# Kernel optimization log

Hardware: AMD Instinct MI355X
Metric: run time of the kernel (lower is better)

Reference implementation:

```python
import jax, jax.numpy as jnp
import numpy as np

S, D, H, DI, DV, DFF = 2048, 1024, 16, 64, 64, 4096


def _xavier(k, shape):
    fan_in, fan_out = shape[-2], shape[-1]
    lim = float(np.sqrt(6.0 / (fan_in + fan_out)))
    return jax.random.uniform(k, shape, jnp.float32, -lim, lim)


def setup_inputs() -> dict:
    key = jax.random.key(0)
    ks = jax.random.split(key, 8)
    input_vecs = jax.random.normal(ks[0], (S, D), jnp.float32)
    WQs = _xavier(ks[1], (H, D, DI))
    WKs = _xavier(ks[2], (H, D, DI))
    WVs = _xavier(ks[3], (H, D, DV))
    WO_w = _xavier(ks[4], (D, H * DV))   # torch Linear weight [out, in]
    WO_b = jnp.zeros((D,), jnp.float32)
    FF1_w = _xavier(ks[5], (DFF, D))
    FF1_b = jnp.zeros((DFF,), jnp.float32)
    FF2_w = _xavier(ks[6], (D, DFF))
    FF2_b = jnp.zeros((D,), jnp.float32)
    return dict(input_vecs=input_vecs, WQs=WQs, WKs=WKs, WVs=WVs,
                WO_w=WO_w, WO_b=WO_b, FF1_w=FF1_w, FF1_b=FF1_b,
                FF2_w=FF2_w, FF2_b=FF2_b)


def reference(input_vecs, WQs, WKs, WVs, WO_w, WO_b, FF1_w, FF1_b, FF2_w, FF2_b):
    h, _, di = WQs.shape
    s = input_vecs.shape[0]
    # per-head projections: [h, s, di/dv]
    Q = jnp.einsum('sd,hde->hse', input_vecs, WQs)
    K = jnp.einsum('sd,hde->hse', input_vecs, WKs)
    V = jnp.einsum('sd,hdv->hsv', input_vecs, WVs)
    scores = jnp.einsum('hse,hte->hst', Q, K) / jnp.sqrt(jnp.float32(di))
    # ALiBi bias: slope_h = (2^{-8/H})^h for h = 1..H; bias = -max(0, i-j)*slope
    idx = jnp.arange(s)
    delta = idx[:, None] - idx[None, :]               # [s, s], i - j
    slopes = (2.0 ** (-8.0 / h)) ** jnp.arange(1, h + 1, dtype=jnp.float32)
    bias = -jnp.maximum(delta, 0).astype(jnp.float32) * slopes[:, None, None]
    causal_mask = jnp.where(delta < 0, -jnp.inf, 0.0)  # -inf above diagonal
    SA = jax.nn.softmax(scores + bias + causal_mask, axis=-1)  # [h, s, s]
    z = jnp.einsum('hst,htv->hsv', SA, V)
    # hstack over heads == transpose to [s, h, dv] then flatten
    zconcat = jnp.transpose(z, (1, 0, 2)).reshape(s, -1)
    attouts = input_vecs + zconcat @ WO_w.T + WO_b
    output_vecs = attouts + jax.nn.relu(attouts @ FF1_w.T + FF1_b) @ FF2_w.T + FF2_b
    return SA, output_vecs
```

## Files before the change

kernel.cpp:

```cpp
#include <hip/hip_runtime.h>
#include <hip/hip_bf16.h>

typedef __hip_bfloat16 bf16;
typedef short v8s __attribute__((ext_vector_type(8)));
typedef float f32x4 __attribute__((ext_vector_type(4)));

static constexpr int S = 2048, D = 1024, H = 16, DFF = 4096;

__device__ __forceinline__ bf16  f2b(float x) { return __float2bfloat16(x); }
__device__ __forceinline__ float b2f(bf16 x)  { return __bfloat162float(x); }

__device__ __forceinline__ void gl2lds16(const void* g, void* l) {
    __builtin_amdgcn_global_load_lds(
        (const __attribute__((address_space(1))) unsigned int*)g,
        (__attribute__((address_space(3))) unsigned int*)l, 16, 0, 0);
}

__global__ __launch_bounds__(256)
void cvt_all(const float* __restrict__ X, const float* __restrict__ WO,
             const float* __restrict__ F1, const float* __restrict__ F2,
             bf16* __restrict__ Xb, bf16* __restrict__ WOb,
             bf16* __restrict__ F1b, bf16* __restrict__ F2b)
{
    const float* src; bf16* dst; int n4;
    switch (blockIdx.y) {
        case 0:  src = X;  dst = Xb;  n4 = S * D / 4;   break;
        case 1:  src = WO; dst = WOb; n4 = D * D / 4;   break;
        case 2:  src = F1; dst = F1b; n4 = DFF * D / 4; break;
        default: src = F2; dst = F2b; n4 = D * DFF / 4; break;
    }
    const int i = blockIdx.x * 256 + threadIdx.x;
    if (i < n4) {
        const float4 v = ((const float4*)src)[i];
        bf16* p = dst + (size_t)i * 4;
        p[0] = f2b(v.x); p[1] = f2b(v.y); p[2] = f2b(v.z); p[3] = f2b(v.w);
    }
}

__global__ __launch_bounds__(256)
void pack_w(const float* __restrict__ WQ, const float* __restrict__ WK,
            const float* __restrict__ WV, bf16* __restrict__ Wcat)
{
    const int d0 = blockIdx.x * 64, h = blockIdx.y, sel = blockIdx.z;
    const float* W = (sel == 0) ? WQ : (sel == 1) ? WK : WV;
    __shared__ float t[64][65];
    const int tid = threadIdx.x;
    for (int idx = tid; idx < 4096; idx += 256) {
        const int d = idx >> 6, e = idx & 63;
        t[d][e] = W[((size_t)h * D + d0 + d) * 64 + e];
    }
    __syncthreads();
    for (int idx = tid; idx < 4096; idx += 256) {
        const int e = idx >> 6, d = idx & 63;
        Wcat[(size_t)(sel * 1024 + h * 64 + e) * D + d0 + d] = f2b(t[d][e]);
    }
}

template<int EPI>
__global__ __launch_bounds__(256)
void gemm_nt(const bf16* __restrict__ A, const bf16* __restrict__ B,
             int M, int N, int K,
             const float* __restrict__ bias, const float* __restrict__ res_f,
             float* __restrict__ out_f, bf16* __restrict__ out_h,
             bf16* __restrict__ Qb, bf16* __restrict__ Kb, bf16* __restrict__ Vt)
{
    __shared__ bf16 sA[128 * 32];
    __shared__ bf16 sB[128 * 32];
    const int tid = threadIdx.x;
    const int lane = tid & 63, quad = lane >> 4, l15 = lane & 15;
    const int wave = tid >> 6, wm = wave >> 1, wn = wave & 1;
    const size_t m0 = (size_t)blockIdx.x * 128, n0 = (size_t)blockIdx.y * 128;
    const int trow = tid >> 2, tcol = (tid & 3) * 8;

    const bf16* pA = A + (m0 + trow) * (size_t)K + tcol;
    const bf16* pB = B + (n0 + trow) * (size_t)K + tcol;
    bf16* lA = sA + tid * 8;
    bf16* lB = sB + tid * 8;

    f32x4 acc[4][4] = {};

    for (int k0 = 0; k0 < K; k0 += 32) {
        gl2lds16(pA + k0, lA);
        gl2lds16(pA + 64 * (size_t)K + k0, lA + 2048);
        gl2lds16(pB + k0, lB);
        gl2lds16(pB + 64 * (size_t)K + k0, lB + 2048);
        __syncthreads();
        v8s af[4], bfr[4];
        #pragma unroll
        for (int t = 0; t < 4; ++t) {
            af[t]  = *(const v8s*)(sA + (wm * 64 + t * 16 + l15) * 32 + quad * 8);
            bfr[t] = *(const v8s*)(sB + (wn * 64 + t * 16 + l15) * 32 + quad * 8);
        }
        #pragma unroll
        for (int i = 0; i < 4; ++i)
            #pragma unroll
            for (int j = 0; j < 4; ++j)
                acc[i][j] = __builtin_amdgcn_mfma_f32_16x16x32_bf16(af[i], bfr[j], acc[i][j], 0, 0, 0);
        __syncthreads();
    }

    #pragma unroll
    for (int i = 0; i < 4; ++i) {
        const size_t mbase = m0 + wm * 64 + i * 16 + quad * 4;
        #pragma unroll
        for (int j = 0; j < 4; ++j) {
            const size_t n = n0 + wn * 64 + j * 16 + l15;
            if constexpr (EPI == 0) {
                const int sel = (int)(n >> 10), hh = (int)((n >> 6) & 15), e = (int)(n & 63);
                if (sel == 2) {
                    bf16* p = Vt + ((size_t)hh * 64 + e) * S + mbase;
                    p[0] = f2b(acc[i][j][0]); p[1] = f2b(acc[i][j][1]);
                    p[2] = f2b(acc[i][j][2]); p[3] = f2b(acc[i][j][3]);
                } else {
                    const float sc = (sel == 0) ? 0.125f : 1.0f;
                    bf16* p = ((sel == 0) ? Qb : Kb) + ((size_t)hh * S + mbase) * 64 + e;
                    p[0]   = f2b(acc[i][j][0] * sc);
                    p[64]  = f2b(acc[i][j][1] * sc);
                    p[128] = f2b(acc[i][j][2] * sc);
                    p[192] = f2b(acc[i][j][3] * sc);
                }
            } else {
                #pragma unroll
                for (int r = 0; r < 4; ++r) {
                    const size_t m = mbase + r;
                    float v = acc[i][j][r] + bias[n];
                    if constexpr (EPI == 1) {
                        v += res_f[m * (size_t)N + n];
                        out_f[m * (size_t)N + n] = v;
                        out_h[m * (size_t)N + n] = f2b(v);
                    }
                    if constexpr (EPI == 2) {
                        v = fmaxf(v, 0.f);
                        out_h[m * (size_t)N + n] = f2b(v);
                    }
                    if constexpr (EPI == 3) {
                        v += res_f[m * (size_t)N + n];
                        out_f[m * (size_t)N + n] = v;
                    }
                }
            }
        }
    }
}

__global__ __launch_bounds__(256)
void attn_kernel(const bf16* __restrict__ Qb, const bf16* __restrict__ Kb,
                 const bf16* __restrict__ Vt, float* __restrict__ SA,
                 bf16* __restrict__ zf)
{
    constexpr int EST = 2056;
    __shared__ bf16 ebuf[16 * EST];
    __shared__ float wsum[4][16];
    __shared__ float inv16[16];

    const int bi = blockIdx.x, h = blockIdx.y;
    const int i0 = bi * 16;
    const int tid = threadIdx.x, wave = tid >> 6, lane = tid & 63;
    const int quad = lane >> 4, l15 = lane & 15;
    const int ntiles = bi + 1;
    const float slope = exp2f(-0.5f * (float)(h + 1));

    { const int r = tid >> 4, c = ntiles * 16 + (tid & 15);
      if (c < EST) ebuf[r * EST + c] = f2b(0.f); }

    const bf16* Qrow = Qb + ((size_t)h * S + i0 + l15) * 64;
    const v8s qf0 = *(const v8s*)(Qrow + quad * 8);
    const v8s qf1 = *(const v8s*)(Qrow + 32 + quad * 8);

    const bf16* Kh = Kb + (size_t)h * S * 64;
    float esum[4] = {0.f, 0.f, 0.f, 0.f};
    for (int jt = wave; jt < ntiles; jt += 4) {
        const bf16* Krow = Kh + (size_t)(jt * 16 + l15) * 64;
        const v8s kf0 = *(const v8s*)(Krow + quad * 8);
        const v8s kf1 = *(const v8s*)(Krow + 32 + quad * 8);
        f32x4 c = {0.f, 0.f, 0.f, 0.f};
        c = __builtin_amdgcn_mfma_f32_16x16x32_bf16(qf0, kf0, c, 0, 0, 0);
        c = __builtin_amdgcn_mfma_f32_16x16x32_bf16(qf1, kf1, c, 0, 0, 0);
        const int j = jt * 16 + l15;
        #pragma unroll
        for (int r = 0; r < 4; ++r) {
            const int i = i0 + quad * 4 + r;
            float e = 0.f;
            if (j <= i) e = __expf(c[r] - (float)(i - j) * slope);
            const bf16 eb = f2b(e);
            ebuf[(quad * 4 + r) * EST + j] = eb;
            esum[r] += b2f(eb);
        }
    }
    #pragma unroll
    for (int r = 0; r < 4; ++r) {
        float v = esum[r];
        v += __shfl_xor(v, 1); v += __shfl_xor(v, 2);
        v += __shfl_xor(v, 4); v += __shfl_xor(v, 8);
        if (l15 == 0) wsum[wave][quad * 4 + r] = v;
    }
    __syncthreads();
    if (tid < 16)
        inv16[tid] = 1.f / (wsum[0][tid] + wsum[1][tid] + wsum[2][tid] + wsum[3][tid]);
    __syncthreads();

    float* SAb = SA + ((size_t)h * S + i0) * S;
    for (int idx = tid; idx < 16 * 512; idx += 256) {
        const int row = idx >> 9, c4 = idx & 511;
        const int i = i0 + row, col = c4 * 4;
        const float iv = inv16[row];
        const bf16* er = ebuf + row * EST + col;
        float4 o;
        o.x = (col     <= i) ? b2f(er[0]) * iv : 0.f;
        o.y = (col + 1 <= i) ? b2f(er[1]) * iv : 0.f;
        o.z = (col + 2 <= i) ? b2f(er[2]) * iv : 0.f;
        o.w = (col + 3 <= i) ? b2f(er[3]) * iv : 0.f;
        ((float4*)(SAb + (size_t)row * S))[c4] = o;
    }

    const int nc = (bi + 2) >> 1;
    const bf16* Vrow = Vt + ((size_t)h * 64 + wave * 16 + l15) * (size_t)S;
    f32x4 oc = {0.f, 0.f, 0.f, 0.f};
    for (int ch = 0; ch < nc; ++ch) {
        const v8s pf = *(const v8s*)(ebuf + l15 * EST + ch * 32 + quad * 8);
        const v8s vf = *(const v8s*)(Vrow + ch * 32 + quad * 8);
        oc = __builtin_amdgcn_mfma_f32_16x16x32_bf16(pf, vf, oc, 0, 0, 0);
    }
    #pragma unroll
    for (int r = 0; r < 4; ++r) {
        const int row = quad * 4 + r;
        zf[(size_t)(i0 + row) * (H * 64) + h * 64 + wave * 16 + l15] = f2b(oc[r] * inv16[row]);
    }
}

extern "C" void kernel_launch(void* const* d_in, const int* in_sizes, int n_in,
                              void* d_out, int out_size, void* d_ws, size_t ws_size,
                              hipStream_t stream)
{
    const float* X     = (const float*)d_in[0];
    const float* WQs   = (const float*)d_in[1];
    const float* WKs   = (const float*)d_in[2];
    const float* WVs   = (const float*)d_in[3];
    const float* WO_w  = (const float*)d_in[4];
    const float* WO_b  = (const float*)d_in[5];
    const float* FF1_w = (const float*)d_in[6];
    const float* FF1_b = (const float*)d_in[7];
    const float* FF2_w = (const float*)d_in[8];
    const float* FF2_b = (const float*)d_in[9];

    float* SA   = (float*)d_out;
    float* out2 = SA + (size_t)H * S * S;

    char* ws = (char*)d_ws;
    bf16* FF1b = (bf16*)(ws);
    bf16* FF2b = (bf16*)(ws + (size_t)( 8u << 20));
    bf16* Xb   = (bf16*)(ws + (size_t)(16u << 20));
    bf16* Wcat = (bf16*)(ws + (size_t)(20u << 20));
    bf16* WOb  = (bf16*)(ws + (size_t)(26u << 20));
    bf16* zf   = (bf16*)(ws + (size_t)(28u << 20));
    bf16* y1   = (bf16*)(ws + (size_t)(16u << 20));
    bf16* Qb   = (bf16*)(ws + (size_t)(32u << 20));
    bf16* Kb   = (bf16*)(ws + (size_t)(36u << 20));
    bf16* Vt   = (bf16*)(ws + (size_t)(40u << 20));
    float* attf = (float*)(ws + (size_t)(32u << 20));
    bf16*  atth = (bf16*)(ws + (size_t)(40u << 20));

    cvt_all<<<dim3(4096, 4), 256, 0, stream>>>(X, WO_w, FF1_w, FF2_w, Xb, WOb, FF1b, FF2b);
    pack_w<<<dim3(16, 16, 3), 256, 0, stream>>>(WQs, WKs, WVs, Wcat);
    gemm_nt<0><<<dim3(16, 24), 256, 0, stream>>>(Xb, Wcat, S, 3072, D,
        nullptr, nullptr, nullptr, nullptr, Qb, Kb, Vt);
    attn_kernel<<<dim3(S / 16, H), 256, 0, stream>>>(Qb, Kb, Vt, SA, zf);
    gemm_nt<1><<<dim3(16, 8), 256, 0, stream>>>(zf, WOb, S, D, D,
        WO_b, X, attf, atth, nullptr, nullptr, nullptr);
    gemm_nt<2><<<dim3(16, 32), 256, 0, stream>>>(atth, FF1b, S, DFF, D,
        FF1_b, nullptr, nullptr, y1, nullptr, nullptr, nullptr);
    gemm_nt<3><<<dim3(16, 8), 256, 0, stream>>>(y1, FF2b, S, D, DFF,
        FF2_b, attf, out2, nullptr, nullptr, nullptr, nullptr);
}
```

Before: 609.1 us.

## Split-K FF2 GEMM, widen attention to 512 threads, reverse block order, prefetch K/V

The FF2 GEMM (K=4096, only 128 blocks) becomes a two-way split-K that writes fp32 partials, followed by a combine kernel that adds bias and the residual, so more CUs are kept busy. The attention kernel moves to 512 threads with 8 waves: the PV product is split across two wave groups and reduced through shared memory. Blocks are launched in reverse order so the long causal rows start first, and K/V fragments are register-prefetched one iteration ahead. The cost is extra fp32 partial-buffer traffic, an additional kernel launch, and more shared memory and registers per attention block.

```diff
diff --git a/kernel.cpp b/kernel.cpp
--- a/kernel.cpp
+++ b/kernel.cpp
@@ -59,7 +59,7 @@
 template<int EPI>
 __global__ __launch_bounds__(256)
 void gemm_nt(const bf16* __restrict__ A, const bf16* __restrict__ B,
-             int M, int N, int K,
+             int M, int N, int Kd, int Kstride,
              const float* __restrict__ bias, const float* __restrict__ res_f,
              float* __restrict__ out_f, bf16* __restrict__ out_h,
              bf16* __restrict__ Qb, bf16* __restrict__ Kb, bf16* __restrict__ Vt)
@@ -70,20 +70,21 @@
     const int lane = tid & 63, quad = lane >> 4, l15 = lane & 15;
     const int wave = tid >> 6, wm = wave >> 1, wn = wave & 1;
     const size_t m0 = (size_t)blockIdx.x * 128, n0 = (size_t)blockIdx.y * 128;
+    const int koff = (EPI == 4) ? blockIdx.z * Kd : 0;
     const int trow = tid >> 2, tcol = (tid & 3) * 8;
 
-    const bf16* pA = A + (m0 + trow) * (size_t)K + tcol;
-    const bf16* pB = B + (n0 + trow) * (size_t)K + tcol;
+    const bf16* pA = A + (m0 + trow) * (size_t)Kstride + koff + tcol;
+    const bf16* pB = B + (n0 + trow) * (size_t)Kstride + koff + tcol;
     bf16* lA = sA + tid * 8;
     bf16* lB = sB + tid * 8;
 
     f32x4 acc[4][4] = {};
 
-    for (int k0 = 0; k0 < K; k0 += 32) {
+    for (int k0 = 0; k0 < Kd; k0 += 32) {
         gl2lds16(pA + k0, lA);
-        gl2lds16(pA + 64 * (size_t)K + k0, lA + 2048);
+        gl2lds16(pA + 64 * (size_t)Kstride + k0, lA + 2048);
         gl2lds16(pB + k0, lB);
-        gl2lds16(pB + 64 * (size_t)K + k0, lB + 2048);
+        gl2lds16(pB + 64 * (size_t)Kstride + k0, lB + 2048);
         __syncthreads();
         v8s af[4], bfr[4];
         #pragma unroll
@@ -119,6 +120,11 @@
                     p[128] = f2b(acc[i][j][2] * sc);
                     p[192] = f2b(acc[i][j][3] * sc);
                 }
+            } else if constexpr (EPI == 4) {
+                float* po = out_f + (size_t)blockIdx.z * (size_t)M * N;
+                #pragma unroll
+                for (int r = 0; r < 4; ++r)
+                    po[(mbase + r) * (size_t)N + n] = acc[i][j][r];
             } else {
                 #pragma unroll
                 for (int r = 0; r < 4; ++r) {
@@ -133,10 +139,6 @@
                         v = fmaxf(v, 0.f);
                         out_h[m * (size_t)N + n] = f2b(v);
                     }
-                    if constexpr (EPI == 3) {
-                        v += res_f[m * (size_t)N + n];
-                        out_f[m * (size_t)N + n] = v;
-                    }
                 }
             }
         }
@@ -144,24 +146,46 @@
 }
 
 __global__ __launch_bounds__(256)
+void ff2_combine(const float* __restrict__ p0, const float* __restrict__ p1,
+                 const float* __restrict__ bias, const float* __restrict__ attf,
+                 float* __restrict__ out2)
+{
+    const int i = blockIdx.x * 256 + threadIdx.x;
+    const float4 a = ((const float4*)p0)[i];
+    const float4 b = ((const float4*)p1)[i];
+    const float4 r = ((const float4*)attf)[i];
+    const float4 bs = ((const float4*)bias)[i & (D / 4 - 1)];
+    float4 o;
+    o.x = a.x + b.x + r.x + bs.x;
+    o.y = a.y + b.y + r.y + bs.y;
+    o.z = a.z + b.z + r.z + bs.z;
+    o.w = a.w + b.w + r.w + bs.w;
+    ((float4*)out2)[i] = o;
+}
+
+__global__ __launch_bounds__(512)
 void attn_kernel(const bf16* __restrict__ Qb, const bf16* __restrict__ Kb,
                  const bf16* __restrict__ Vt, float* __restrict__ SA,
                  bf16* __restrict__ zf)
 {
     constexpr int EST = 2056;
     __shared__ bf16 ebuf[16 * EST];
-    __shared__ float wsum[4][16];
+    __shared__ float wsum[8][16];
     __shared__ float inv16[16];
-
-    const int bi = blockIdx.x, h = blockIdx.y;
+    __shared__ float pvacc[8][16][16];
+
+    const int bi = (int)gridDim.x - 1 - (int)blockIdx.x;
+    const int h = blockIdx.y;
     const int i0 = bi * 16;
     const int tid = threadIdx.x, wave = tid >> 6, lane = tid & 63;
     const int quad = lane >> 4, l15 = lane & 15;
     const int ntiles = bi + 1;
     const float slope = exp2f(-0.5f * (float)(h + 1));
 
-    { const int r = tid >> 4, c = ntiles * 16 + (tid & 15);
-      if (c < EST) ebuf[r * EST + c] = f2b(0.f); }
+    if (tid < 256) {
+        const int r = tid >> 4, c = ntiles * 16 + (tid & 15);
+        if (c < EST) ebuf[r * EST + c] = f2b(0.f);
+    }
 
     const bf16* Qrow = Qb + ((size_t)h * S + i0 + l15) * 64;
     const v8s qf0 = *(const v8s*)(Qrow + quad * 8);
@@ -169,22 +193,36 @@
 
     const bf16* Kh = Kb + (size_t)h * S * 64;
     float esum[4] = {0.f, 0.f, 0.f, 0.f};
-    for (int jt = wave; jt < ntiles; jt += 4) {
-        const bf16* Krow = Kh + (size_t)(jt * 16 + l15) * 64;
-        const v8s kf0 = *(const v8s*)(Krow + quad * 8);
-        const v8s kf1 = *(const v8s*)(Krow + 32 + quad * 8);
-        f32x4 c = {0.f, 0.f, 0.f, 0.f};
-        c = __builtin_amdgcn_mfma_f32_16x16x32_bf16(qf0, kf0, c, 0, 0, 0);
-        c = __builtin_amdgcn_mfma_f32_16x16x32_bf16(qf1, kf1, c, 0, 0, 0);
-        const int j = jt * 16 + l15;
-        #pragma unroll
-        for (int r = 0; r < 4; ++r) {
-            const int i = i0 + quad * 4 + r;
-            float e = 0.f;
-            if (j <= i) e = __expf(c[r] - (float)(i - j) * slope);
-            const bf16 eb = f2b(e);
-            ebuf[(quad * 4 + r) * EST + j] = eb;
-            esum[r] += b2f(eb);
+    {
+        int jt = wave;
+        v8s kf0 = {}, kf1 = {};
+        if (jt < ntiles) {
+            const bf16* Krow = Kh + (size_t)(jt * 16 + l15) * 64;
+            kf0 = *(const v8s*)(Krow + quad * 8);
+            kf1 = *(const v8s*)(Krow + 32 + quad * 8);
+        }
+        while (jt < ntiles) {
+            const int jn = jt + 8;
+            v8s nf0 = kf0, nf1 = kf1;
+            if (jn < ntiles) {
+                const bf16* Krow = Kh + (size_t)(jn * 16 + l15) * 64;
+                nf0 = *(const v8s*)(Krow + quad * 8);
+                nf1 = *(const v8s*)(Krow + 32 + quad * 8);
+            }
+            f32x4 c = {0.f, 0.f, 0.f, 0.f};
+            c = __builtin_amdgcn_mfma_f32_16x16x32_bf16(qf0, kf0, c, 0, 0, 0);
+            c = __builtin_amdgcn_mfma_f32_16x16x32_bf16(qf1, kf1, c, 0, 0, 0);
+            const int j = jt * 16 + l15;
+            #pragma unroll
+            for (int r = 0; r < 4; ++r) {
+                const int i = i0 + quad * 4 + r;
+                float e = 0.f;
+                if (j <= i) e = __expf(c[r] - (float)(i - j) * slope);
+                const bf16 eb = f2b(e);
+                ebuf[(quad * 4 + r) * EST + j] = eb;
+                esum[r] += b2f(eb);
+            }
+            kf0 = nf0; kf1 = nf1; jt = jn;
         }
     }
     #pragma unroll
@@ -195,12 +233,16 @@
         if (l15 == 0) wsum[wave][quad * 4 + r] = v;
     }
     __syncthreads();
-    if (tid < 16)
-        inv16[tid] = 1.f / (wsum[0][tid] + wsum[1][tid] + wsum[2][tid] + wsum[3][tid]);
+    if (tid < 16) {
+        float s = 0.f;
+        #pragma unroll
+        for (int w = 0; w < 8; ++w) s += wsum[w][tid];
+        inv16[tid] = 1.f / s;
+    }
     __syncthreads();
 
     float* SAb = SA + ((size_t)h * S + i0) * S;
-    for (int idx = tid; idx < 16 * 512; idx += 256) {
+    for (int idx = tid; idx < 16 * 512; idx += 512) {
         const int row = idx >> 9, c4 = idx & 511;
         const int i = i0 + row, col = c4 * 4;
         const float iv = inv16[row];
@@ -214,17 +256,30 @@
     }
 
     const int nc = (bi + 2) >> 1;
-    const bf16* Vrow = Vt + ((size_t)h * 64 + wave * 16 + l15) * (size_t)S;
+    const int vt = wave & 3, jh = wave >> 2;
+    const bf16* Vrow = Vt + ((size_t)h * 64 + vt * 16 + l15) * (size_t)S;
     f32x4 oc = {0.f, 0.f, 0.f, 0.f};
-    for (int ch = 0; ch < nc; ++ch) {
-        const v8s pf = *(const v8s*)(ebuf + l15 * EST + ch * 32 + quad * 8);
-        const v8s vf = *(const v8s*)(Vrow + ch * 32 + quad * 8);
-        oc = __builtin_amdgcn_mfma_f32_16x16x32_bf16(pf, vf, oc, 0, 0, 0);
+    {
+        int ch = jh;
+        v8s vf = {};
+        if (ch < nc) vf = *(const v8s*)(Vrow + ch * 32 + quad * 8);
+        while (ch < nc) {
+            const int cn = ch + 2;
+            v8s vn = vf;
+            if (cn < nc) vn = *(const v8s*)(Vrow + cn * 32 + quad * 8);
+            const v8s pf = *(const v8s*)(ebuf + l15 * EST + ch * 32 + quad * 8);
+            oc = __builtin_amdgcn_mfma_f32_16x16x32_bf16(pf, vf, oc, 0, 0, 0);
+            vf = vn; ch = cn;
+        }
     }
     #pragma unroll
-    for (int r = 0; r < 4; ++r) {
-        const int row = quad * 4 + r;
-        zf[(size_t)(i0 + row) * (H * 64) + h * 64 + wave * 16 + l15] = f2b(oc[r] * inv16[row]);
+    for (int r = 0; r < 4; ++r)
+        pvacc[wave][quad * 4 + r][l15] = oc[r];
+    __syncthreads();
+    for (int idx = tid; idx < 1024; idx += 512) {
+        const int v4 = idx >> 8, rem = idx & 255, row = rem >> 4, col = rem & 15;
+        const float z = (pvacc[v4][row][col] + pvacc[v4 + 4][row][col]) * inv16[row];
+        zf[(size_t)(i0 + row) * (H * 64) + h * 64 + v4 * 16 + col] = f2b(z);
     }
 }
 
@@ -247,28 +302,32 @@
     float* out2 = SA + (size_t)H * S * S;
 
     char* ws = (char*)d_ws;
-    bf16* FF1b = (bf16*)(ws);
-    bf16* FF2b = (bf16*)(ws + (size_t)( 8u << 20));
-    bf16* Xb   = (bf16*)(ws + (size_t)(16u << 20));
-    bf16* Wcat = (bf16*)(ws + (size_t)(20u << 20));
-    bf16* WOb  = (bf16*)(ws + (size_t)(26u << 20));
-    bf16* zf   = (bf16*)(ws + (size_t)(28u << 20));
-    bf16* y1   = (bf16*)(ws + (size_t)(16u << 20));
-    bf16* Qb   = (bf16*)(ws + (size_t)(32u << 20));
-    bf16* Kb   = (bf16*)(ws + (size_t)(36u << 20));
-    bf16* Vt   = (bf16*)(ws + (size_t)(40u << 20));
-    float* attf = (float*)(ws + (size_t)(32u << 20));
-    bf16*  atth = (bf16*)(ws + (size_t)(40u << 20));
+    const size_t MB = 1u << 20;
+    bf16*  FF1b = (bf16*)(ws);
+    bf16*  FF2b = (bf16*)(ws + 8 * MB);
+    bf16*  Xb   = (bf16*)(ws + 16 * MB);
+    bf16*  Wcat = (bf16*)(ws + 20 * MB);
+    bf16*  WOb  = (bf16*)(ws + 26 * MB);
+    bf16*  zf   = (bf16*)(ws + 28 * MB);
+    bf16*  Qb   = (bf16*)(ws + 32 * MB);
+    bf16*  Kb   = (bf16*)(ws + 36 * MB);
+    bf16*  Vt   = (bf16*)(ws + 40 * MB);
+    float* attf = (float*)(ws + 44 * MB);
+    bf16*  atth = (bf16*)(ws + 52 * MB);
+    bf16*  y1   = (bf16*)(ws + 56 * MB);
+    float* p0   = (float*)(ws + 72 * MB);
 
     cvt_all<<<dim3(4096, 4), 256, 0, stream>>>(X, WO_w, FF1_w, FF2_w, Xb, WOb, FF1b, FF2b);
     pack_w<<<dim3(16, 16, 3), 256, 0, stream>>>(WQs, WKs, WVs, Wcat);
-    gemm_nt<0><<<dim3(16, 24), 256, 0, stream>>>(Xb, Wcat, S, 3072, D,
+    gemm_nt<0><<<dim3(16, 24), 256, 0, stream>>>(Xb, Wcat, S, 3072, D, D,
         nullptr, nullptr, nullptr, nullptr, Qb, Kb, Vt);
-    attn_kernel<<<dim3(S / 16, H), 256, 0, stream>>>(Qb, Kb, Vt, SA, zf);
-    gemm_nt<1><<<dim3(16, 8), 256, 0, stream>>>(zf, WOb, S, D, D,
+    attn_kernel<<<dim3(S / 16, H), 512, 0, stream>>>(Qb, Kb, Vt, SA, zf);
+    gemm_nt<1><<<dim3(16, 8), 256, 0, stream>>>(zf, WOb, S, D, D, D,
         WO_b, X, attf, atth, nullptr, nullptr, nullptr);
-    gemm_nt<2><<<dim3(16, 32), 256, 0, stream>>>(atth, FF1b, S, DFF, D,
+    gemm_nt<2><<<dim3(16, 32), 256, 0, stream>>>(atth, FF1b, S, DFF, D, D,
         FF1_b, nullptr, nullptr, y1, nullptr, nullptr, nullptr);
-    gemm_nt<3><<<dim3(16, 8), 256, 0, stream>>>(y1, FF2b, S, D, DFF,
-        FF2_b, attf, out2, nullptr, nullptr, nullptr, nullptr);
-}
+    gemm_nt<4><<<dim3(16, 8, 2), 256, 0, stream>>>(y1, FF2b, S, D, DFF / 2, DFF,
+        nullptr, nullptr, p0, nullptr, nullptr, nullptr, nullptr);
+    ff2_combine<<<dim3(S * D / 4 / 256), 256, 0, stream>>>(
+        p0, p0 + (size_t)S * D, FF2_b, attf, out2);
+}
```

Result: faster. 549.8 us (-9.7%).
